# Kernel tuning notes

Hardware: AMD Instinct MI355X
Metric: run time of the kernel (lower is better)

## Reference

```python
import jax, jax.numpy as jnp
import numpy as np

V, E, H, S = 50257, 1024, 1024, 2048


def setup_inputs() -> dict:
    key = jax.random.key(0)
    ks = jax.random.split(key, 24)
    def n(k, shape, s=0.02):
        return jax.random.normal(k, shape, dtype=jnp.float32) * s
    inp = {
        "x": jax.random.normal(ks[0], (1, E), dtype=jnp.float32),
        "encoder_outputs": jax.random.normal(ks[1], (S, 2 * H), dtype=jnp.float32),
        "sentence": jax.random.randint(ks[2], (S,), 0, V, dtype=jnp.int32).at[0].set(7),
        "prev_probs": jax.random.uniform(ks[3], (V + S,), dtype=jnp.float32),
        "h0": n(ks[4], (1, H), 1.0),
        "c0": n(ks[5], (1, H), 1.0),
        "attn_W": n(ks[6], (S, 2 * H)), "attn_b": jnp.zeros((S,), jnp.float32),
        "comb_W": n(ks[7], (H, 2 * H)), "comb_b": jnp.zeros((H,), jnp.float32),
        "Ws_W": n(ks[8], (H, 2 * H)), "Ws_b": jnp.zeros((H,), jnp.float32),
        "Wo_W": n(ks[9], (V, H)), "Wo_b": jnp.zeros((V,), jnp.float32),
        "Wc_W": n(ks[10], (H, 2 * H)), "Wc_b": jnp.zeros((H,), jnp.float32),
        "W_ih": n(ks[11], (4 * H, E + 2 * H)), "W_hh": n(ks[12], (4 * H, H)),
        "b_ih": jnp.zeros((4 * H,), jnp.float32), "b_hh": jnp.zeros((4 * H,), jnp.float32),
        "prev_word": 7,
    }
    return inp


def reference(x, encoder_outputs, sentence, prev_probs, h0, c0,
              attn_W, attn_b, comb_W, comb_b, Ws_W, Ws_b,
              Wo_W, Wo_b, Wc_W, Wc_b, W_ih, W_hh, b_ih, b_hh, prev_word):
    xe, h, c = x[0], h0[0], c0[0]            # [E], [H], [H]
    # attentive read: attention over encoder positions, then combine to [H]
    att_logits = jnp.concatenate([xe, h]) @ attn_W.T + attn_b      # [S]
    attn_w = jax.nn.softmax(att_logits)
    ctx = attn_w @ encoder_outputs                                 # [2H]
    attentive = ctx @ comb_W.T + comb_b                            # [H]
    # selective read (copy mechanism): positions where sentence == prev_word
    probs_c = prev_probs[V:]                                       # [S]
    rho = jnp.where(sentence == prev_word, probs_c, 0.0)
    rho = rho / (rho.sum() + 1e-9)
    selective = (rho @ encoder_outputs) @ Ws_W.T + Ws_b            # [H]
    # single LSTM step (PyTorch gate order i,f,g,o)
    lstm_in = jnp.concatenate([xe, selective, attentive])          # [E+2H]
    gates = lstm_in @ W_ih.T + b_ih + h @ W_hh.T + b_hh            # [4H]
    i, f, g, o = jnp.split(gates, 4)
    c1 = jax.nn.sigmoid(f) * c + jax.nn.sigmoid(i) * jnp.tanh(g)
    h1 = jax.nn.sigmoid(o) * jnp.tanh(c1)                          # [H]
    # generate + copy scores, joint softmax
    score_g = h1 @ Wo_W.T + Wo_b                                   # [V]
    score_c = jnp.tanh(encoder_outputs @ Wc_W.T + Wc_b) @ h1       # [S]
    probs = jax.nn.softmax(jnp.concatenate([score_g, score_c]))    # [V+S]
    return probs, h1[None, :], c1[None, :]
```

## Files before the change

kernel.cpp:

```cpp
#include <hip/hip_runtime.h>
#include <hip/hip_bf16.h>
#include <math.h>

#define VV 50257
#define EE 1024
#define HH 1024
#define SS 2048
#define VS (VV + SS)

#define OFF_LOGA   0
#define OFF_ATTW   2048
#define OFF_RHO    4096
#define OFF_CTX    6144
#define OFF_SEL    8192
#define OFF_LSTMIN 10240
#define OFF_GATES  13312
#define OFF_H1     17408
#define OFF_LOG    18432
#define OFF_MS     70784
#define OFF_LS     70912
#define OFF_G      71040
#define OFF_T0     71168
#define OFF_T1     (71168 + 2048*1024)

typedef __attribute__((ext_vector_type(8))) short bf16x8;
typedef __attribute__((ext_vector_type(4))) float f32x4;

__device__ inline float wave_reduce(float v) {
    #pragma unroll
    for (int off = 32; off > 0; off >>= 1) v += __shfl_down(v, off, 64);
    return v;
}

__device__ inline unsigned short f2bf(float f) {
    unsigned int u = __builtin_bit_cast(unsigned int, f);
    u += 0x7FFFu + ((u >> 16) & 1u);
    return (unsigned short)(u >> 16);
}

__global__ void k_attn_logits(const float* __restrict__ x, const float* __restrict__ h0,
                              const float* __restrict__ attn_W, const float* __restrict__ attn_b,
                              float* __restrict__ out) {
    int wave = (blockIdx.x * blockDim.x + threadIdx.x) >> 6;
    int lane = threadIdx.x & 63;
    if (wave >= SS) return;
    const float4* rp = (const float4*)(attn_W + (size_t)wave * 2048);
    float acc = 0.f;
    #pragma unroll
    for (int k = 0; k < 8; ++k) {
        int idx = lane + 64 * k;
        float4 w = rp[idx];
        int j = idx * 4;
        const float* cat = (j < 1024) ? (x + j) : (h0 + (j - 1024));
        acc += w.x * cat[0] + w.y * cat[1] + w.z * cat[2] + w.w * cat[3];
    }
    acc = wave_reduce(acc);
    if (lane == 0) out[wave] = acc + attn_b[wave];
}

__global__ void k_prep(const float* __restrict__ logits, const int* __restrict__ sentence,
                       const float* __restrict__ prev_probs, const int* __restrict__ prev_word,
                       const float* __restrict__ x,
                       float* __restrict__ attn_w, float* __restrict__ rho,
                       float* __restrict__ lstm_in, float* __restrict__ ctxsel) {
    __shared__ float red[256];
    int tid = threadIdx.x;
    for (int j = tid; j < 4096; j += 256) ctxsel[j] = 0.f;
    float m = -1e30f;
    for (int s = tid; s < SS; s += 256) m = fmaxf(m, logits[s]);
    red[tid] = m; __syncthreads();
    for (int o = 128; o > 0; o >>= 1) { if (tid < o) red[tid] = fmaxf(red[tid], red[tid + o]); __syncthreads(); }
    m = red[0]; __syncthreads();
    float sum = 0.f;
    for (int s = tid; s < SS; s += 256) sum += expf(logits[s] - m);
    red[tid] = sum; __syncthreads();
    for (int o = 128; o > 0; o >>= 1) { if (tid < o) red[tid] += red[tid + o]; __syncthreads(); }
    float inv = 1.f / red[0]; __syncthreads();
    for (int s = tid; s < SS; s += 256) attn_w[s] = expf(logits[s] - m) * inv;
    int pw = prev_word[0];
    float rsum = 0.f;
    for (int s = tid; s < SS; s += 256) rsum += (sentence[s] == pw) ? prev_probs[VV + s] : 0.f;
    red[tid] = rsum; __syncthreads();
    for (int o = 128; o > 0; o >>= 1) { if (tid < o) red[tid] += red[tid + o]; __syncthreads(); }
    float rinv = 1.f / (red[0] + 1e-9f); __syncthreads();
    for (int s = tid; s < SS; s += 256) rho[s] = ((sentence[s] == pw) ? prev_probs[VV + s] : 0.f) * rinv;
    for (int j = tid; j < EE; j += 256) lstm_in[j] = x[j];
}

__global__ void k_ctx(const float* __restrict__ enc, const float* __restrict__ attn_w,
                      const float* __restrict__ rho, float* __restrict__ ctx,
                      float* __restrict__ selctx) {
    int col4 = blockIdx.x * 256 + threadIdx.x;
    int s0 = blockIdx.y * 64;
    float4 a = {0.f, 0.f, 0.f, 0.f}, r = {0.f, 0.f, 0.f, 0.f};
    const float4* p = (const float4*)enc + (size_t)s0 * 512 + col4;
    #pragma unroll 4
    for (int i = 0; i < 64; ++i) {
        float4 v = p[(size_t)i * 512];
        float w = attn_w[s0 + i], q = rho[s0 + i];
        a.x += w * v.x; a.y += w * v.y; a.z += w * v.z; a.w += w * v.w;
        r.x += q * v.x; r.y += q * v.y; r.z += q * v.z; r.w += q * v.w;
    }
    int c = col4 * 4;
    atomicAdd(&ctx[c], a.x); atomicAdd(&ctx[c+1], a.y); atomicAdd(&ctx[c+2], a.z); atomicAdd(&ctx[c+3], a.w);
    atomicAdd(&selctx[c], r.x); atomicAdd(&selctx[c+1], r.y); atomicAdd(&selctx[c+2], r.z); atomicAdd(&selctx[c+3], r.w);
}

__global__ void k_comb(const float* __restrict__ ctx, const float* __restrict__ selctx,
                       const float* __restrict__ comb_W, const float* __restrict__ comb_b,
                       const float* __restrict__ Ws_W, const float* __restrict__ Ws_b,
                       float* __restrict__ lstm_in) {
    int wave = (blockIdx.x * blockDim.x + threadIdx.x) >> 6;
    int lane = threadIdx.x & 63;
    if (wave >= 2048) return;
    bool sel = wave >= 1024;
    int i = sel ? wave - 1024 : wave;
    const float4* rp = (const float4*)((sel ? Ws_W : comb_W) + (size_t)i * 2048);
    const float4* vp = (const float4*)(sel ? selctx : ctx);
    float acc = 0.f;
    #pragma unroll
    for (int k = 0; k < 8; ++k) {
        int idx = lane + 64 * k;
        float4 w = rp[idx]; float4 v = vp[idx];
        acc += w.x * v.x + w.y * v.y + w.z * v.z + w.w * v.w;
    }
    acc = wave_reduce(acc);
    if (lane == 0) lstm_in[sel ? (1024 + i) : (2048 + i)] = acc + (sel ? Ws_b[i] : comb_b[i]);
}

__global__ __launch_bounds__(256) void k_gates_gemm(
        const float* __restrict__ lstm_in, const float* __restrict__ h0,
        const float* __restrict__ W_ih, const float* __restrict__ W_hh,
        const float* __restrict__ b_ih, const float* __restrict__ b_hh,
        float* __restrict__ gates,
        const float* __restrict__ A,
        const float* __restrict__ B,
        float* __restrict__ T0, float* __restrict__ T1) {
    __shared__ unsigned short As[128 * 32];
    __shared__ unsigned short Bs[128 * 32];
    int tid = threadIdx.x;
    if (blockIdx.x < 1024) {
        int wave = (blockIdx.x * 256 + tid) >> 6;
        int lane = tid & 63;
        const float4* rp = (const float4*)(W_ih + (size_t)wave * 3072);
        const float4* vp = (const float4*)lstm_in;
        float acc = 0.f;
        #pragma unroll
        for (int k = 0; k < 12; ++k) {
            int idx = lane + 64 * k;
            float4 w = rp[idx]; float4 v = vp[idx];
            acc += w.x * v.x + w.y * v.y + w.z * v.z + w.w * v.w;
        }
        const float4* hp = (const float4*)(W_hh + (size_t)wave * 1024);
        const float4* h4 = (const float4*)h0;
        #pragma unroll
        for (int k = 0; k < 4; ++k) {
            int idx = lane + 64 * k;
            float4 w = hp[idx]; float4 v = h4[idx];
            acc += w.x * v.x + w.y * v.y + w.z * v.z + w.w * v.w;
        }
        acc = wave_reduce(acc);
        if (lane == 0) gates[wave] = acc + b_ih[wave] + b_hh[wave];
        return;
    }
    int gg = blockIdx.x - 1024;
    int sK = gg >> 7;
    int rem = gg & 127;
    int mbase = (rem >> 3) * 128;
    int nbase = (rem & 7) * 128;
    float* C = sK ? T1 : T0;
    int lane = tid & 63;
    int wid = tid >> 6;
    int wm = (wid >> 1) * 64;
    int wn = (wid & 1) * 64;
    int lrow = lane & 15;
    int lk = (lane >> 4) * 8;
    f32x4 acc[4][4] = {};
    int kbeg = sK * 1024;
    for (int k0 = kbeg; k0 < kbeg + 1024; k0 += 32) {
        #pragma unroll
        for (int i = 0; i < 4; ++i) {
            int fi = tid + 256 * i;
            int row = fi >> 3;
            int kg = fi & 7;
            float4 v = *(const float4*)(A + (size_t)(mbase + row) * 2048 + k0 + kg * 4);
            ushort4 a4 = { f2bf(v.x), f2bf(v.y), f2bf(v.z), f2bf(v.w) };
            *(ushort4*)(As + row * 32 + kg * 4) = a4;
            float4 w = *(const float4*)(B + (size_t)(nbase + row) * 2048 + k0 + kg * 4);
            ushort4 b4 = { f2bf(w.x), f2bf(w.y), f2bf(w.z), f2bf(w.w) };
            *(ushort4*)(Bs + row * 32 + kg * 4) = b4;
        }
        __syncthreads();
        bf16x8 af[4], bfr[4];
        #pragma unroll
        for (int t = 0; t < 4; ++t) {
            af[t]  = *(const bf16x8*)(As + (wm + t * 16 + lrow) * 32 + lk);
            bfr[t] = *(const bf16x8*)(Bs + (wn + t * 16 + lrow) * 32 + lk);
        }
        #pragma unroll
        for (int mt = 0; mt < 4; ++mt)
            #pragma unroll
            for (int nt = 0; nt < 4; ++nt)
                acc[mt][nt] = __builtin_amdgcn_mfma_f32_16x16x32_bf16(af[mt], bfr[nt], acc[mt][nt], 0, 0, 0);
        __syncthreads();
    }
    int crow0 = (lane >> 4) * 4;
    int ccol = lane & 15;
    #pragma unroll
    for (int mt = 0; mt < 4; ++mt)
        #pragma unroll
        for (int nt = 0; nt < 4; ++nt) {
            int col = nbase + wn + nt * 16 + ccol;
            #pragma unroll
            for (int r = 0; r < 4; ++r) {
                int row = mbase + wm + mt * 16 + crow0 + r;
                C[(size_t)row * 1024 + col] = acc[mt][nt][r];
            }
        }
}

__global__ void k_lstm(const float* __restrict__ gates, const float* __restrict__ c0,
                       float* __restrict__ out, float* __restrict__ h1ws) {
    int k = blockIdx.x * 256 + threadIdx.x;
    float ig = gates[k], fg = gates[1024 + k], gg = gates[2048 + k], og = gates[3072 + k];
    float si = 1.f / (1.f + expf(-ig));
    float sf = 1.f / (1.f + expf(-fg));
    float so = 1.f / (1.f + expf(-og));
    float c1 = sf * c0[k] + si * tanhf(gg);
    float h1 = so * tanhf(c1);
    out[VS + k] = h1;
    out[VS + 1024 + k] = c1;
    h1ws[k] = h1;
}

__global__ void k_scores(const float* __restrict__ Wo_W, const float* __restrict__ Wo_b,
                         const float* __restrict__ T0, const float* __restrict__ T1,
                         const float* __restrict__ Wc_b,
                         const float* __restrict__ h1, float* __restrict__ logits) {
    int wave = (blockIdx.x * blockDim.x + threadIdx.x) >> 6;
    int lane = threadIdx.x & 63;
    if (wave >= VS) return;
    const float4* hp = (const float4*)h1;
    float acc = 0.f;
    if (wave < VV) {
        const float4* rp = (const float4*)(Wo_W + (size_t)wave * 1024);
        #pragma unroll
        for (int k = 0; k < 4; ++k) {
            int idx = lane + 64 * k;
            float4 w = rp[idx]; float4 v = hp[idx];
            acc += w.x * v.x + w.y * v.y + w.z * v.z + w.w * v.w;
        }
        acc = wave_reduce(acc);
        if (lane == 0) logits[wave] = acc + Wo_b[wave];
    } else {
        int r = wave - VV;
        const float4* p0 = (const float4*)(T0 + (size_t)r * 1024);
        const float4* p1 = (const float4*)(T1 + (size_t)r * 1024);
        const float4* bp = (const float4*)Wc_b;
        #pragma unroll
        for (int k = 0; k < 4; ++k) {
            int idx = lane + 64 * k;
            float4 a0 = p0[idx]; float4 a1 = p1[idx]; float4 bb = bp[idx]; float4 v = hp[idx];
            acc += tanhf(a0.x + a1.x + bb.x) * v.x + tanhf(a0.y + a1.y + bb.y) * v.y
                 + tanhf(a0.z + a1.z + bb.z) * v.z + tanhf(a0.w + a1.w + bb.w) * v.w;
        }
        acc = wave_reduce(acc);
        if (lane == 0) logits[wave] = acc;
    }
}

__global__ void k_sm1(const float* __restrict__ logits, float* __restrict__ ms, float* __restrict__ ls) {
    __shared__ float rm[256], rl[256];
    int tid = threadIdx.x;
    float m = -1e30f, l = 0.f;
    for (int v = blockIdx.x * 256 + tid; v < VS; v += 128 * 256) {
        float x = logits[v];
        float nm = fmaxf(m, x);
        l = l * expf(m - nm) + expf(x - nm);
        m = nm;
    }
    rm[tid] = m; rl[tid] = l; __syncthreads();
    for (int o = 128; o > 0; o >>= 1) {
        if (tid < o) {
            float m2 = rm[tid + o], l2 = rl[tid + o];
            float nm = fmaxf(rm[tid], m2);
            rl[tid] = rl[tid] * expf(rm[tid] - nm) + l2 * expf(m2 - nm);
            rm[tid] = nm;
        }
        __syncthreads();
    }
    if (tid == 0) { ms[blockIdx.x] = rm[0]; ls[blockIdx.x] = rl[0]; }
}

__global__ void k_sm2(const float* __restrict__ ms, const float* __restrict__ ls, float* __restrict__ g) {
    __shared__ float rm[128], rl[128];
    int tid = threadIdx.x;
    rm[tid] = ms[tid]; rl[tid] = ls[tid]; __syncthreads();
    for (int o = 64; o > 0; o >>= 1) {
        if (tid < o) {
            float m2 = rm[tid + o], l2 = rl[tid + o];
            float nm = fmaxf(rm[tid], m2);
            rl[tid] = rl[tid] * expf(rm[tid] - nm) + l2 * expf(m2 - nm);
            rm[tid] = nm;
        }
        __syncthreads();
    }
    if (tid == 0) { g[0] = rm[0]; g[1] = 1.f / rl[0]; }
}

__global__ void k_sm3(const float* __restrict__ logits, const float* __restrict__ g,
                      float* __restrict__ out) {
    int v = blockIdx.x * 256 + threadIdx.x;
    if (v < VS) out[v] = expf(logits[v] - g[0]) * g[1];
}

extern "C" void kernel_launch(void* const* d_in, const int* in_sizes, int n_in,
                              void* d_out, int out_size, void* d_ws, size_t ws_size,
                              hipStream_t stream) {
    (void)in_sizes; (void)n_in; (void)out_size; (void)ws_size;
    const float* x          = (const float*)d_in[0];
    const float* enc        = (const float*)d_in[1];
    const int*   sentence   = (const int*)d_in[2];
    const float* prev_probs = (const float*)d_in[3];
    const float* h0         = (const float*)d_in[4];
    const float* c0         = (const float*)d_in[5];
    const float* attn_W     = (const float*)d_in[6];
    const float* attn_b     = (const float*)d_in[7];
    const float* comb_W     = (const float*)d_in[8];
    const float* comb_b     = (const float*)d_in[9];
    const float* Ws_W       = (const float*)d_in[10];
    const float* Ws_b       = (const float*)d_in[11];
    const float* Wo_W       = (const float*)d_in[12];
    const float* Wo_b       = (const float*)d_in[13];
    const float* Wc_W       = (const float*)d_in[14];
    const float* Wc_b       = (const float*)d_in[15];
    const float* W_ih       = (const float*)d_in[16];
    const float* W_hh       = (const float*)d_in[17];
    const float* b_ih       = (const float*)d_in[18];
    const float* b_hh       = (const float*)d_in[19];
    const int*   prev_word  = (const int*)d_in[20];
    float* ws  = (float*)d_ws;
    float* out = (float*)d_out;

    k_attn_logits<<<512, 256, 0, stream>>>(x, h0, attn_W, attn_b, ws + OFF_LOGA);
    k_prep<<<1, 256, 0, stream>>>(ws + OFF_LOGA, sentence, prev_probs, prev_word, x,
                                  ws + OFF_ATTW, ws + OFF_RHO, ws + OFF_LSTMIN, ws + OFF_CTX);
    k_ctx<<<dim3(2, 32), 256, 0, stream>>>(enc, ws + OFF_ATTW, ws + OFF_RHO,
                                           ws + OFF_CTX, ws + OFF_SEL);
    k_comb<<<512, 256, 0, stream>>>(ws + OFF_CTX, ws + OFF_SEL, comb_W, comb_b,
                                    Ws_W, Ws_b, ws + OFF_LSTMIN);
    k_gates_gemm<<<1280, 256, 0, stream>>>(ws + OFF_LSTMIN, h0, W_ih, W_hh, b_ih, b_hh,
                                           ws + OFF_GATES, enc, Wc_W,
                                           ws + OFF_T0, ws + OFF_T1);
    k_lstm<<<4, 256, 0, stream>>>(ws + OFF_GATES, c0, out, ws + OFF_H1);
    k_scores<<<13077, 256, 0, stream>>>(Wo_W, Wo_b, ws + OFF_T0, ws + OFF_T1, Wc_b,
                                        ws + OFF_H1, ws + OFF_LOG);
    k_sm1<<<128, 256, 0, stream>>>(ws + OFF_LOG, ws + OFF_MS, ws + OFF_LS);
    k_sm2<<<1, 128, 0, stream>>>(ws + OFF_MS, ws + OFF_LS, ws + OFF_G);
    k_sm3<<<205, 256, 0, stream>>>(ws + OFF_LOG, ws + OFF_G, out);
}
```

Before: 478.6 us.

## Fuse launch pipeline, pre-convert GEMM operands to bf16, fold softmax into scores

Cuts the launch count from ten to six. Attention logits, zeroing and input copies are merged into one front kernel. The attention softmax and rho computation move into the ctx kernel, which each block recomputes redundantly. The LSTM cell update is folded into the scores kernel, and the scores kernel now uses a grid-stride loop and produces per-block online-softmax partials, so the separate max/sum passes are dropped. The encoder and Wc matrices are converted to bf16 once up front, so the GEMM loads 16-byte bf16 vectors instead of converting fp32 on every tile. The cost is an extra conversion pass with its own writes, redundant softmax work in every block, and the LSTM math repeated in every scores block.

```diff
diff --git a/kernel.cpp b/kernel.cpp
--- a/kernel.cpp
+++ b/kernel.cpp
@@ -8,22 +8,23 @@
 #define SS 2048
 #define VS (VV + SS)
 
+#define NSCB 2048
+
 #define OFF_LOGA   0
-#define OFF_ATTW   2048
-#define OFF_RHO    4096
-#define OFF_CTX    6144
-#define OFF_SEL    8192
-#define OFF_LSTMIN 10240
-#define OFF_GATES  13312
-#define OFF_H1     17408
-#define OFF_LOG    18432
-#define OFF_MS     70784
-#define OFF_LS     70912
-#define OFF_G      71040
-#define OFF_T0     71168
-#define OFF_T1     (71168 + 2048*1024)
+#define OFF_CTX    2048
+#define OFF_SEL    4096
+#define OFF_LSTMIN 6144
+#define OFF_GATES  9216
+#define OFF_LOG    13312
+#define OFF_MS     65664
+#define OFF_LS     67712
+#define OFF_T0     69760
+#define OFF_T1     (69760 + 2048*1024)
+#define OFF_ENCB   (OFF_T1 + 2048*1024)
+#define OFF_WCB    (OFF_ENCB + 2048*1024)
 
 typedef __attribute__((ext_vector_type(8))) short bf16x8;
+typedef __attribute__((ext_vector_type(8))) unsigned short u16x8;
 typedef __attribute__((ext_vector_type(4))) float f32x4;
 
 __device__ inline float wave_reduce(float v) {
@@ -38,66 +39,91 @@
     return (unsigned short)(u >> 16);
 }
 
-__global__ void k_attn_logits(const float* __restrict__ x, const float* __restrict__ h0,
-                              const float* __restrict__ attn_W, const float* __restrict__ attn_b,
-                              float* __restrict__ out) {
-    int wave = (blockIdx.x * blockDim.x + threadIdx.x) >> 6;
-    int lane = threadIdx.x & 63;
-    if (wave >= SS) return;
-    const float4* rp = (const float4*)(attn_W + (size_t)wave * 2048);
-    float acc = 0.f;
-    #pragma unroll
-    for (int k = 0; k < 8; ++k) {
-        int idx = lane + 64 * k;
-        float4 w = rp[idx];
-        int j = idx * 4;
-        const float* cat = (j < 1024) ? (x + j) : (h0 + (j - 1024));
-        acc += w.x * cat[0] + w.y * cat[1] + w.z * cat[2] + w.w * cat[3];
-    }
-    acc = wave_reduce(acc);
-    if (lane == 0) out[wave] = acc + attn_b[wave];
-}
-
-__global__ void k_prep(const float* __restrict__ logits, const int* __restrict__ sentence,
-                       const float* __restrict__ prev_probs, const int* __restrict__ prev_word,
-                       const float* __restrict__ x,
-                       float* __restrict__ attn_w, float* __restrict__ rho,
-                       float* __restrict__ lstm_in, float* __restrict__ ctxsel) {
+__global__ __launch_bounds__(256) void k_front(
+        const float* __restrict__ x, const float* __restrict__ h0,
+        const float* __restrict__ attn_W, const float* __restrict__ attn_b,
+        float* __restrict__ loga,
+        const float* __restrict__ enc, const float* __restrict__ Wc_W,
+        unsigned short* __restrict__ encb, unsigned short* __restrict__ Wcb,
+        float* __restrict__ ctxsel, float* __restrict__ lstm_in) {
+    int bx = blockIdx.x, tid = threadIdx.x;
+    if (bx < 512) {
+        int wave = (bx * 256 + tid) >> 6;
+        int lane = tid & 63;
+        const float4* rp = (const float4*)(attn_W + (size_t)wave * 2048);
+        float acc = 0.f;
+        #pragma unroll
+        for (int k = 0; k < 8; ++k) {
+            int idx = lane + 64 * k;
+            float4 w = rp[idx];
+            int j = idx * 4;
+            const float* cat = (j < 1024) ? (x + j) : (h0 + (j - 1024));
+            acc += w.x * cat[0] + w.y * cat[1] + w.z * cat[2] + w.w * cat[3];
+        }
+        acc = wave_reduce(acc);
+        if (lane == 0) loga[wave] = acc + attn_b[wave];
+        return;
+    }
+    if (bx < 1280) {
+        bool isenc = bx < 1024;
+        int b = isenc ? bx - 512 : bx - 1024;
+        const float* src = isenc ? enc : Wc_W;
+        unsigned short* dst = isenc ? encb : Wcb;
+        size_t base = (size_t)b * 8192;
+        #pragma unroll
+        for (int p = 0; p < 8; ++p) {
+            size_t idx = base + p * 1024 + tid * 4;
+            float4 v = *(const float4*)(src + idx);
+            ushort4 o = { f2bf(v.x), f2bf(v.y), f2bf(v.z), f2bf(v.w) };
+            *(ushort4*)(dst + idx) = o;
+        }
+        return;
+    }
+    if (bx == 1280) {
+        for (int j = tid; j < 4096; j += 256) ctxsel[j] = 0.f;
+        return;
+    }
+    for (int j = tid; j < EE; j += 256) lstm_in[j] = x[j];
+}
+
+__global__ __launch_bounds__(256) void k_ctx(
+        const float* __restrict__ enc, const float* __restrict__ logits,
+        const int* __restrict__ sentence, const float* __restrict__ prev_probs,
+        const int* __restrict__ prev_word,
+        float* __restrict__ ctx, float* __restrict__ selctx) {
     __shared__ float red[256];
+    __shared__ float aw[64], rh[64];
     int tid = threadIdx.x;
-    for (int j = tid; j < 4096; j += 256) ctxsel[j] = 0.f;
     float m = -1e30f;
     for (int s = tid; s < SS; s += 256) m = fmaxf(m, logits[s]);
     red[tid] = m; __syncthreads();
     for (int o = 128; o > 0; o >>= 1) { if (tid < o) red[tid] = fmaxf(red[tid], red[tid + o]); __syncthreads(); }
     m = red[0]; __syncthreads();
     float sum = 0.f;
-    for (int s = tid; s < SS; s += 256) sum += expf(logits[s] - m);
+    for (int s = tid; s < SS; s += 256) sum += __expf(logits[s] - m);
     red[tid] = sum; __syncthreads();
     for (int o = 128; o > 0; o >>= 1) { if (tid < o) red[tid] += red[tid + o]; __syncthreads(); }
     float inv = 1.f / red[0]; __syncthreads();
-    for (int s = tid; s < SS; s += 256) attn_w[s] = expf(logits[s] - m) * inv;
     int pw = prev_word[0];
     float rsum = 0.f;
     for (int s = tid; s < SS; s += 256) rsum += (sentence[s] == pw) ? prev_probs[VV + s] : 0.f;
     red[tid] = rsum; __syncthreads();
     for (int o = 128; o > 0; o >>= 1) { if (tid < o) red[tid] += red[tid + o]; __syncthreads(); }
     float rinv = 1.f / (red[0] + 1e-9f); __syncthreads();
-    for (int s = tid; s < SS; s += 256) rho[s] = ((sentence[s] == pw) ? prev_probs[VV + s] : 0.f) * rinv;
-    for (int j = tid; j < EE; j += 256) lstm_in[j] = x[j];
-}
-
-__global__ void k_ctx(const float* __restrict__ enc, const float* __restrict__ attn_w,
-                      const float* __restrict__ rho, float* __restrict__ ctx,
-                      float* __restrict__ selctx) {
-    int col4 = blockIdx.x * 256 + threadIdx.x;
     int s0 = blockIdx.y * 64;
+    if (tid < 64) {
+        int s = s0 + tid;
+        aw[tid] = __expf(logits[s] - m) * inv;
+        rh[tid] = ((sentence[s] == pw) ? prev_probs[VV + s] : 0.f) * rinv;
+    }
+    __syncthreads();
+    int col4 = blockIdx.x * 256 + tid;
     float4 a = {0.f, 0.f, 0.f, 0.f}, r = {0.f, 0.f, 0.f, 0.f};
     const float4* p = (const float4*)enc + (size_t)s0 * 512 + col4;
     #pragma unroll 4
     for (int i = 0; i < 64; ++i) {
         float4 v = p[(size_t)i * 512];
-        float w = attn_w[s0 + i], q = rho[s0 + i];
+        float w = aw[i], q = rh[i];
         a.x += w * v.x; a.y += w * v.y; a.z += w * v.z; a.w += w * v.w;
         r.x += q * v.x; r.y += q * v.y; r.z += q * v.z; r.w += q * v.w;
     }
@@ -106,13 +132,13 @@
     atomicAdd(&selctx[c], r.x); atomicAdd(&selctx[c+1], r.y); atomicAdd(&selctx[c+2], r.z); atomicAdd(&selctx[c+3], r.w);
 }
 
-__global__ void k_comb(const float* __restrict__ ctx, const float* __restrict__ selctx,
-                       const float* __restrict__ comb_W, const float* __restrict__ comb_b,
-                       const float* __restrict__ Ws_W, const float* __restrict__ Ws_b,
-                       float* __restrict__ lstm_in) {
+__global__ __launch_bounds__(256) void k_comb(
+        const float* __restrict__ ctx, const float* __restrict__ selctx,
+        const float* __restrict__ comb_W, const float* __restrict__ comb_b,
+        const float* __restrict__ Ws_W, const float* __restrict__ Ws_b,
+        float* __restrict__ lstm_in) {
     int wave = (blockIdx.x * blockDim.x + threadIdx.x) >> 6;
     int lane = threadIdx.x & 63;
-    if (wave >= 2048) return;
     bool sel = wave >= 1024;
     int i = sel ? wave - 1024 : wave;
     const float4* rp = (const float4*)((sel ? Ws_W : comb_W) + (size_t)i * 2048);
@@ -133,11 +159,11 @@
         const float* __restrict__ W_ih, const float* __restrict__ W_hh,
         const float* __restrict__ b_ih, const float* __restrict__ b_hh,
         float* __restrict__ gates,
-        const float* __restrict__ A,
-        const float* __restrict__ B,
+        const unsigned short* __restrict__ Ab,
+        const unsigned short* __restrict__ Bb,
         float* __restrict__ T0, float* __restrict__ T1) {
-    __shared__ unsigned short As[128 * 32];
-    __shared__ unsigned short Bs[128 * 32];
+    __shared__ __attribute__((aligned(16))) unsigned short As[128 * 32];
+    __shared__ __attribute__((aligned(16))) unsigned short Bs[128 * 32];
     int tid = threadIdx.x;
     if (blockIdx.x < 1024) {
         int wave = (blockIdx.x * 256 + tid) >> 6;
@@ -179,16 +205,14 @@
     int kbeg = sK * 1024;
     for (int k0 = kbeg; k0 < kbeg + 1024; k0 += 32) {
         #pragma unroll
-        for (int i = 0; i < 4; ++i) {
-            int fi = tid + 256 * i;
-            int row = fi >> 3;
-            int kg = fi & 7;
-            float4 v = *(const float4*)(A + (size_t)(mbase + row) * 2048 + k0 + kg * 4);
-            ushort4 a4 = { f2bf(v.x), f2bf(v.y), f2bf(v.z), f2bf(v.w) };
-            *(ushort4*)(As + row * 32 + kg * 4) = a4;
-            float4 w = *(const float4*)(B + (size_t)(nbase + row) * 2048 + k0 + kg * 4);
-            ushort4 b4 = { f2bf(w.x), f2bf(w.y), f2bf(w.z), f2bf(w.w) };
-            *(ushort4*)(Bs + row * 32 + kg * 4) = b4;
+        for (int p = 0; p < 2; ++p) {
+            int fi = p * 256 + tid;
+            int row = fi >> 2;
+            int c8 = fi & 3;
+            *(u16x8*)(As + row * 32 + c8 * 8) =
+                *(const u16x8*)(Ab + (size_t)(mbase + row) * 2048 + k0 + c8 * 8);
+            *(u16x8*)(Bs + row * 32 + c8 * 8) =
+                *(const u16x8*)(Bb + (size_t)(nbase + row) * 2048 + k0 + c8 * 8);
         }
         __syncthreads();
         bf16x8 af[4], bfr[4];
@@ -219,64 +243,89 @@
         }
 }
 
-__global__ void k_lstm(const float* __restrict__ gates, const float* __restrict__ c0,
-                       float* __restrict__ out, float* __restrict__ h1ws) {
-    int k = blockIdx.x * 256 + threadIdx.x;
-    float ig = gates[k], fg = gates[1024 + k], gg = gates[2048 + k], og = gates[3072 + k];
-    float si = 1.f / (1.f + expf(-ig));
-    float sf = 1.f / (1.f + expf(-fg));
-    float so = 1.f / (1.f + expf(-og));
-    float c1 = sf * c0[k] + si * tanhf(gg);
-    float h1 = so * tanhf(c1);
-    out[VS + k] = h1;
-    out[VS + 1024 + k] = c1;
-    h1ws[k] = h1;
-}
-
-__global__ void k_scores(const float* __restrict__ Wo_W, const float* __restrict__ Wo_b,
-                         const float* __restrict__ T0, const float* __restrict__ T1,
-                         const float* __restrict__ Wc_b,
-                         const float* __restrict__ h1, float* __restrict__ logits) {
-    int wave = (blockIdx.x * blockDim.x + threadIdx.x) >> 6;
-    int lane = threadIdx.x & 63;
-    if (wave >= VS) return;
-    const float4* hp = (const float4*)h1;
-    float acc = 0.f;
-    if (wave < VV) {
-        const float4* rp = (const float4*)(Wo_W + (size_t)wave * 1024);
-        #pragma unroll
-        for (int k = 0; k < 4; ++k) {
-            int idx = lane + 64 * k;
-            float4 w = rp[idx]; float4 v = hp[idx];
-            acc += w.x * v.x + w.y * v.y + w.z * v.z + w.w * v.w;
+__global__ __launch_bounds__(256) void k_scores(
+        const float* __restrict__ gates, const float* __restrict__ c0,
+        const float* __restrict__ Wo_W, const float* __restrict__ Wo_b,
+        const float* __restrict__ T0, const float* __restrict__ T1,
+        const float* __restrict__ Wc_b,
+        float* __restrict__ logits, float* __restrict__ out,
+        float* __restrict__ ms, float* __restrict__ ls) {
+    __shared__ float h1s[1024];
+    __shared__ float wm_s[4], wl_s[4];
+    int tid = threadIdx.x, bid = blockIdx.x;
+    #pragma unroll
+    for (int kk = 0; kk < 4; ++kk) {
+        int j = tid + 256 * kk;
+        float ig = gates[j], fg = gates[1024 + j], gg = gates[2048 + j], og = gates[3072 + j];
+        float si = 1.f / (1.f + __expf(-ig));
+        float sf = 1.f / (1.f + __expf(-fg));
+        float so = 1.f / (1.f + __expf(-og));
+        float c1 = sf * c0[j] + si * tanhf(gg);
+        float h1 = so * tanhf(c1);
+        h1s[j] = h1;
+        if (bid == 0) { out[VS + j] = h1; out[VS + 1024 + j] = c1; }
+    }
+    __syncthreads();
+    int lane = tid & 63, wid = tid >> 6;
+    int gw = bid * 4 + wid;
+    float m = -1e30f, l = 0.f;
+    const float4* hp = (const float4*)h1s;
+    for (int v = gw; v < VS; v += NSCB * 4) {
+        float acc = 0.f;
+        if (v < VV) {
+            const float4* rp = (const float4*)(Wo_W + (size_t)v * 1024);
+            #pragma unroll
+            for (int k = 0; k < 4; ++k) {
+                int idx = lane + 64 * k;
+                float4 w = rp[idx]; float4 hv = hp[idx];
+                acc += w.x * hv.x + w.y * hv.y + w.z * hv.z + w.w * hv.w;
+            }
+        } else {
+            int r = v - VV;
+            const float4* p0 = (const float4*)(T0 + (size_t)r * 1024);
+            const float4* p1 = (const float4*)(T1 + (size_t)r * 1024);
+            const float4* bp = (const float4*)Wc_b;
+            #pragma unroll
+            for (int k = 0; k < 4; ++k) {
+                int idx = lane + 64 * k;
+                float4 a0 = p0[idx], a1 = p1[idx], bb = bp[idx], hv = hp[idx];
+                acc += tanhf(a0.x + a1.x + bb.x) * hv.x + tanhf(a0.y + a1.y + bb.y) * hv.y
+                     + tanhf(a0.z + a1.z + bb.z) * hv.z + tanhf(a0.w + a1.w + bb.w) * hv.w;
+            }
         }
         acc = wave_reduce(acc);
-        if (lane == 0) logits[wave] = acc + Wo_b[wave];
-    } else {
-        int r = wave - VV;
-        const float4* p0 = (const float4*)(T0 + (size_t)r * 1024);
-        const float4* p1 = (const float4*)(T1 + (size_t)r * 1024);
-        const float4* bp = (const float4*)Wc_b;
-        #pragma unroll
-        for (int k = 0; k < 4; ++k) {
-            int idx = lane + 64 * k;
-            float4 a0 = p0[idx]; float4 a1 = p1[idx]; float4 bb = bp[idx]; float4 v = hp[idx];
-            acc += tanhf(a0.x + a1.x + bb.x) * v.x + tanhf(a0.y + a1.y + bb.y) * v.y
-                 + tanhf(a0.z + a1.z + bb.z) * v.z + tanhf(a0.w + a1.w + bb.w) * v.w;
-        }
-        acc = wave_reduce(acc);
-        if (lane == 0) logits[wave] = acc;
-    }
-}
-
-__global__ void k_sm1(const float* __restrict__ logits, float* __restrict__ ms, float* __restrict__ ls) {
+        if (lane == 0) {
+            float lg = acc + (v < VV ? Wo_b[v] : 0.f);
+            logits[v] = lg;
+            float nm = fmaxf(m, lg);
+            l = l * __expf(m - nm) + __expf(lg - nm);
+            m = nm;
+        }
+    }
+    if (lane == 0) { wm_s[wid] = m; wl_s[wid] = l; }
+    __syncthreads();
+    if (tid == 0) {
+        float M = wm_s[0], L = wl_s[0];
+        #pragma unroll
+        for (int w = 1; w < 4; ++w) {
+            float nm = fmaxf(M, wm_s[w]);
+            L = L * __expf(M - nm) + wl_s[w] * __expf(wm_s[w] - nm);
+            M = nm;
+        }
+        ms[bid] = M; ls[bid] = L;
+    }
+}
+
+__global__ __launch_bounds__(256) void k_smfinal(
+        const float* __restrict__ ms, const float* __restrict__ ls,
+        const float* __restrict__ logits, float* __restrict__ out) {
     __shared__ float rm[256], rl[256];
     int tid = threadIdx.x;
     float m = -1e30f, l = 0.f;
-    for (int v = blockIdx.x * 256 + tid; v < VS; v += 128 * 256) {
-        float x = logits[v];
-        float nm = fmaxf(m, x);
-        l = l * expf(m - nm) + expf(x - nm);
+    for (int i = tid; i < NSCB; i += 256) {
+        float bm = ms[i], bl = ls[i];
+        float nm = fmaxf(m, bm);
+        l = l * __expf(m - nm) + bl * __expf(bm - nm);
         m = nm;
     }
     rm[tid] = m; rl[tid] = l; __syncthreads();
@@ -284,34 +333,14 @@
         if (tid < o) {
             float m2 = rm[tid + o], l2 = rl[tid + o];
             float nm = fmaxf(rm[tid], m2);
-            rl[tid] = rl[tid] * expf(rm[tid] - nm) + l2 * expf(m2 - nm);
+            rl[tid] = rl[tid] * __expf(rm[tid] - nm) + l2 * __expf(m2 - nm);
             rm[tid] = nm;
         }
         __syncthreads();
     }
-    if (tid == 0) { ms[blockIdx.x] = rm[0]; ls[blockIdx.x] = rl[0]; }
-}
-
-__global__ void k_sm2(const float* __restrict__ ms, const float* __restrict__ ls, float* __restrict__ g) {
-    __shared__ float rm[128], rl[128];
-    int tid = threadIdx.x;
-    rm[tid] = ms[tid]; rl[tid] = ls[tid]; __syncthreads();
-    for (int o = 64; o > 0; o >>= 1) {
-        if (tid < o) {
-            float m2 = rm[tid + o], l2 = rl[tid + o];
-            float nm = fmaxf(rm[tid], m2);
-            rl[tid] = rl[tid] * expf(rm[tid] - nm) + l2 * expf(m2 - nm);
-            rm[tid] = nm;
-        }
-        __syncthreads();
-    }
-    if (tid == 0) { g[0] = rm[0]; g[1] = 1.f / rl[0]; }
-}
-
-__global__ void k_sm3(const float* __restrict__ logits, const float* __restrict__ g,
-                      float* __restrict__ out) {
-    int v = blockIdx.x * 256 + threadIdx.x;
-    if (v < VS) out[v] = expf(logits[v] - g[0]) * g[1];
+    float M = rm[0], Linv = 1.f / rl[0];
+    for (int v = blockIdx.x * 256 + tid; v < VS; v += 128 * 256)
+        out[v] = __expf(logits[v] - M) * Linv;
 }
 
 extern "C" void kernel_launch(void* const* d_in, const int* in_sizes, int n_in,
@@ -341,21 +370,21 @@
     const int*   prev_word  = (const int*)d_in[20];
     float* ws  = (float*)d_ws;
     float* out = (float*)d_out;
-
-    k_attn_logits<<<512, 256, 0, stream>>>(x, h0, attn_W, attn_b, ws + OFF_LOGA);
-    k_prep<<<1, 256, 0, stream>>>(ws + OFF_LOGA, sentence, prev_probs, prev_word, x,
-                                  ws + OFF_ATTW, ws + OFF_RHO, ws + OFF_LSTMIN, ws + OFF_CTX);
-    k_ctx<<<dim3(2, 32), 256, 0, stream>>>(enc, ws + OFF_ATTW, ws + OFF_RHO,
-                                           ws + OFF_CTX, ws + OFF_SEL);
+    unsigned short* encb = (unsigned short*)(ws + OFF_ENCB);
+    unsigned short* Wcb  = (unsigned short*)(ws + OFF_WCB);
+
+    k_front<<<1282, 256, 0, stream>>>(x, h0, attn_W, attn_b, ws + OFF_LOGA,
+                                      enc, Wc_W, encb, Wcb,
+                                      ws + OFF_CTX, ws + OFF_LSTMIN);
+    k_ctx<<<dim3(2, 32), 256, 0, stream>>>(enc, ws + OFF_LOGA, sentence, prev_probs,
+                                           prev_word, ws + OFF_CTX, ws + OFF_SEL);
     k_comb<<<512, 256, 0, stream>>>(ws + OFF_CTX, ws + OFF_SEL, comb_W, comb_b,
                                     Ws_W, Ws_b, ws + OFF_LSTMIN);
     k_gates_gemm<<<1280, 256, 0, stream>>>(ws + OFF_LSTMIN, h0, W_ih, W_hh, b_ih, b_hh,
-                                           ws + OFF_GATES, enc, Wc_W,
+                                           ws + OFF_GATES, encb, Wcb,
                                            ws + OFF_T0, ws + OFF_T1);
-    k_lstm<<<4, 256, 0, stream>>>(ws + OFF_GATES, c0, out, ws + OFF_H1);
-    k_scores<<<13077, 256, 0, stream>>>(Wo_W, Wo_b, ws + OFF_T0, ws + OFF_T1, Wc_b,
-                                        ws + OFF_H1, ws + OFF_LOG);
-    k_sm1<<<128, 256, 0, stream>>>(ws + OFF_LOG, ws + OFF_MS, ws + OFF_LS);
-    k_sm2<<<1, 128, 0, stream>>>(ws + OFF_MS, ws + OFF_LS, ws + OFF_G);
-    k_sm3<<<205, 256, 0, stream>>>(ws + OFF_LOG, ws + OFF_G, out);
-}
+    k_scores<<<NSCB, 256, 0, stream>>>(ws + OFF_GATES, c0, Wo_W, Wo_b,
+                                       ws + OFF_T0, ws + OFF_T1, Wc_b,
+                                       ws + OFF_LOG, out, ws + OFF_MS, ws + OFF_LS);
+    k_smfinal<<<128, 256, 0, stream>>>(ws + OFF_MS, ws + OFF_LS, ws + OFF_LOG, out);
+}
```

Result: faster. 451.9 us (-5.6%).
